# Kernel tuning notes

Measured on AMD Instinct MI355X. Metric: run time of the kernel, lower is better.

## Reference

```python
import jax, jax.numpy as jnp
import numpy as np

B, TX, DA, DS, H = 64, 2048, 256, 256, 50

def setup_inputs() -> dict:
    key = jax.random.key(0)
    k1, k2, k3, k4 = jax.random.split(key, 4)
    a = jax.random.normal(k1, (B, TX, DA), dtype=jnp.float32)
    s = jax.random.normal(k2, (B, DS), dtype=jnp.float32)
    # Dense(50, relu) params on concat dim (DA+DS)
    W1 = jax.random.normal(k3, (DA + DS, H), dtype=jnp.float32) / np.sqrt(DA + DS)
    b1 = jnp.zeros((H,), dtype=jnp.float32)
    # Dense(1, tanh) params
    W2 = jax.random.normal(k4, (H, 1), dtype=jnp.float32) / np.sqrt(H)
    b2 = jnp.zeros((1,), dtype=jnp.float32)
    return {"a": a, "s": s, "W1": W1, "b1": b1, "W2": W2, "b2": b2}

def reference(a, s, W1, b1, W2, b2):
    # repeat s along time: [B, Tx, Ds]
    s_rep = jnp.broadcast_to(s[:, None, :], (a.shape[0], a.shape[1], s.shape[-1]))
    x = jnp.concatenate([a, s_rep], axis=-1)              # [B, Tx, Da+Ds]
    h = jax.nn.relu(jnp.einsum('btc,ch->bth', x, W1) + b1)  # [B, Tx, 50]
    e = jnp.tanh(jnp.einsum('bth,ho->bto', h, W2) + b2)     # [B, Tx, 1]
    alphas = jax.nn.softmax(e, axis=1)                     # softmax over time
    # Dot(axes=1): contract the time axis -> [B, 1, Da]
    context = jnp.einsum('bto,btd->bod', alphas, a)
    return context
```

## Files before the change

### kernel.cpp

```cpp
#include <hip/hip_runtime.h>

#define B_ 64
#define TX_ 2048
#define DA_ 256
#define DS_ 256
#define H_ 50

typedef __attribute__((ext_vector_type(4))) float f32x4;
typedef __attribute__((ext_vector_type(8))) short short8;

__device__ __forceinline__ unsigned short f2bf(float x) {
  unsigned int u = __builtin_bit_cast(unsigned int, x);
  u += 0x7FFFu + ((u >> 16) & 1u);
  return (unsigned short)(u >> 16);
}
__device__ __forceinline__ float bf2f(unsigned short h) {
  unsigned int u = ((unsigned int)h) << 16;
  return __builtin_bit_cast(float, u);
}

#define WS_NUM 0
#define WS_DEN 16384
#define WS_C   16448
#define WS_W2  20544
#define WS_B   20608

__global__ __launch_bounds__(256) void prep_kernel(
    const float* __restrict__ s, const float* __restrict__ W1,
    const float* __restrict__ b1, const float* __restrict__ W2,
    float* __restrict__ ws)
{
  const int b = blockIdx.x;
  const int t = threadIdx.x;
  float* num = ws + WS_NUM;
  float* den = ws + WS_DEN;
  float* cws = ws + WS_C;
  float* w2p = ws + WS_W2;
  unsigned short* wsB = (unsigned short*)(ws + WS_B);

  num[b * 256 + t] = 0.0f;
  if (t == 0) den[b] = 0.0f;

  {
    const int h4 = t >> 2, kq = t & 3;
    float cp = 0.0f;
    if (h4 < H_) {
      const float* srow = s + b * DS_;
      #pragma unroll 8
      for (int k = kq * 64; k < kq * 64 + 64; ++k)
        cp += srow[k] * W1[(size_t)(DA_ + k) * H_ + h4];
    }
    cp += __shfl_down(cp, 1);
    cp += __shfl_down(cp, 2);
    if (kq == 0) cws[b * 64 + h4] = (h4 < H_) ? (cp + b1[h4]) : 0.0f;
  }
  if (b == 0 && t < 64) w2p[t] = (t < H_) ? W2[t] : 0.0f;

  #pragma unroll
  for (int ii = 0; ii < 2; ++ii) {
    const int idx = (b * 256 + t) * 2 + ii;
    const int j = idx & 7;
    const int l = (idx >> 3) & 63;
    const int nt = (idx >> 9) & 3;
    const int term = (idx >> 11) & 1;
    const int c = idx >> 12;
    const int k = c * 32 + (l >> 4) * 8 + j;
    const int n = nt * 16 + (l & 15);
    const float wv = (n < H_) ? W1[(size_t)k * H_ + n] : 0.0f;
    const unsigned short hi = f2bf(wv);
    const unsigned short val = term == 0 ? hi : f2bf(wv - bf2f(hi));
    wsB[((size_t)((c * 2 + term) * 4 + nt)) * 512 + l * 8 + j] = val;
  }
}

__global__ __launch_bounds__(256) void fused_kernel(
    const float* __restrict__ a, const float* __restrict__ ws_f,
    const float* __restrict__ b2, float* __restrict__ num,
    float* __restrict__ den)
{
  __shared__ float tile[16384];
  __shared__ float w_sh[64];

  const int t = threadIdx.x;
  const int l = t & 63;
  const int w = __builtin_amdgcn_readfirstlane(t >> 6);
  const int blk = blockIdx.x;
  const int b = blk >> 5;
  const long R0 = (long)blk * 64;

  const float* cws = ws_f + WS_C;
  const float* w2p = ws_f + WS_W2;
  const unsigned short* wsB = (const unsigned short*)(ws_f + WS_B);

  float cv[4], w2v[4];
  #pragma unroll
  for (int nt = 0; nt < 4; ++nt) {
    const int n = nt * 16 + (l & 15);
    cv[nt] = cws[b * 64 + n];
    w2v[nt] = w2p[n];
  }
  const float b2v = b2[0];

  #define STAGE(c)                                                             \
    {                                                                          \
      _Pragma("unroll")                                                        \
      for (int i = 0; i < 2; ++i) {                                            \
        const int slot = w * 2 + i;                                            \
        const int row = slot * 8 + (l >> 3);                                   \
        const long gbyte = (R0 + row) * 1024 + (c) * 128 +                     \
                           (((l & 7) ^ ((l >> 3) & 7)) * 16);                  \
        __builtin_amdgcn_global_load_lds(                                      \
            (const __attribute__((address_space(1))) void*)((const char*)a +   \
                                                            gbyte),            \
            (__attribute__((address_space(3))) void*)&tile[(c)*2048 +          \
                                                           slot * 256],        \
            16, 0, 0);                                                         \
      }                                                                        \
    }

  STAGE(0);
  STAGE(1);

  short8 Bh[2][4], Bl[2][4];
  {
    const short8* Bp = (const short8*)wsB;
    #pragma unroll
    for (int nt = 0; nt < 4; ++nt) {
      Bh[0][nt] = Bp[nt * 64 + l];
      Bl[0][nt] = Bp[(4 + nt) * 64 + l];
    }
  }

  f32x4 acc[4];
  #pragma unroll
  for (int nt = 0; nt < 4; ++nt) acc[nt] = (f32x4){0.f, 0.f, 0.f, 0.f};

  #pragma unroll
  for (int c = 0; c < 8; ++c) {
    if (c + 2 < 8) STAGE(c + 2);
    if (c + 1 < 8) {
      const short8* Bp = (const short8*)(wsB + (size_t)(c + 1) * 4096);
      #pragma unroll
      for (int nt = 0; nt < 4; ++nt) {
        Bh[(c + 1) & 1][nt] = Bp[nt * 64 + l];
        Bl[(c + 1) & 1][nt] = Bp[(4 + nt) * 64 + l];
      }
    }
    if (c < 6)       asm volatile("s_waitcnt vmcnt(10)" ::: "memory");
    else if (c == 6) asm volatile("s_waitcnt vmcnt(8)" ::: "memory");
    else             asm volatile("s_waitcnt vmcnt(0)" ::: "memory");
    __builtin_amdgcn_sched_barrier(0);

    const int row = w * 16 + (l & 15);
    const int mask = (l & 7) << 4;
    const int obase = (l >> 4) * 32;
    const char* tb = (const char*)tile + (size_t)c * 8192 + row * 128;
    const float4 v0 = *(const float4*)(tb + (obase ^ mask));
    const float4 v1 = *(const float4*)(tb + ((obase + 16) ^ mask));
    float av[8] = {v0.x, v0.y, v0.z, v0.w, v1.x, v1.y, v1.z, v1.w};
    short8 Ah, Al;
    #pragma unroll
    for (int j = 0; j < 8; ++j) {
      const unsigned short hi = f2bf(av[j]);
      Ah[j] = (short)hi;
      Al[j] = (short)f2bf(av[j] - bf2f(hi));
    }

    #pragma unroll
    for (int nt = 0; nt < 4; ++nt) {
      acc[nt] = __builtin_amdgcn_mfma_f32_16x16x32_bf16(Ah, Bh[c & 1][nt], acc[nt], 0, 0, 0);
      acc[nt] = __builtin_amdgcn_mfma_f32_16x16x32_bf16(Ah, Bl[c & 1][nt], acc[nt], 0, 0, 0);
      acc[nt] = __builtin_amdgcn_mfma_f32_16x16x32_bf16(Al, Bh[c & 1][nt], acc[nt], 0, 0, 0);
    }
  }

  #pragma unroll
  for (int r = 0; r < 4; ++r) {
    float e = 0.0f;
    #pragma unroll
    for (int nt = 0; nt < 4; ++nt)
      e += fmaxf(acc[nt][r] + cv[nt], 0.0f) * w2v[nt];
    e += __shfl_xor(e, 1);
    e += __shfl_xor(e, 2);
    e += __shfl_xor(e, 4);
    e += __shfl_xor(e, 8);
    if ((l & 15) == 0)
      w_sh[w * 16 + (l >> 4) * 4 + r] = __expf(tanhf(e + b2v));
  }
  __syncthreads();

  if (t < 64) {
    float v = w_sh[t];
    #pragma unroll
    for (int off = 32; off > 0; off >>= 1) v += __shfl_xor(v, off);
    if (t == 0) atomicAdd(&den[b], v);
  }

  {
    const int cc = t >> 5, col = t & 31;
    const char* tb = (const char*)tile + (size_t)cc * 8192;
    float sum = 0.0f;
    #pragma unroll 8
    for (int r = 0; r < 64; ++r) {
      const float av = *(const float*)(tb + r * 128 + ((col * 4) ^ ((r & 7) << 4)));
      sum += w_sh[r] * av;
    }
    atomicAdd(&num[b * 256 + t], sum);
  }
  #undef STAGE
}

__global__ __launch_bounds__(256) void finish_kernel(
    const float* __restrict__ ws_f, float* __restrict__ out)
{
  const int b = blockIdx.x;
  const int t = threadIdx.x;
  out[b * 256 + t] = ws_f[WS_NUM + b * 256 + t] / ws_f[WS_DEN + b];
}

extern "C" void kernel_launch(void* const* d_in, const int* in_sizes, int n_in,
                              void* d_out, int out_size, void* d_ws, size_t ws_size,
                              hipStream_t stream) {
  const float* a  = (const float*)d_in[0];
  const float* s  = (const float*)d_in[1];
  const float* W1 = (const float*)d_in[2];
  const float* b1 = (const float*)d_in[3];
  const float* W2 = (const float*)d_in[4];
  const float* b2 = (const float*)d_in[5];
  float* out = (float*)d_out;
  float* ws  = (float*)d_ws;

  prep_kernel<<<dim3(B_), dim3(256), 0, stream>>>(s, W1, b1, W2, ws);
  fused_kernel<<<dim3(2048), dim3(256), 0, stream>>>(
      a, ws, b2, ws + WS_NUM, ws + WS_DEN);
  finish_kernel<<<dim3(B_), dim3(256), 0, stream>>>(ws, out);
}
```

Baseline: 56.83 us.

## Shrink LDS footprint with a double-buffered ring and bf16 context tile for occupancy

Replaces the full 64KB fp32 tile of `a` with a two-slot staging ring and a separate bf16 copy of the tile (the rounded high halves). That copy is reused for the weighted time-sum. Launch bounds now request 3 blocks per CU. The context reduction becomes per-wave partial sums combined through LDS, and tanh is computed via exp. Prefetch depth drops from two chunks ahead to one, and the context now uses bf16-rounded activations, which lowers accuracy.

```diff
diff --git a/kernel.cpp b/kernel.cpp
--- a/kernel.cpp
+++ b/kernel.cpp
@@ -17,6 +17,15 @@
 __device__ __forceinline__ float bf2f(unsigned short h) {
   unsigned int u = ((unsigned int)h) << 16;
   return __builtin_bit_cast(float, u);
+}
+__device__ __forceinline__ unsigned bitf(float x) {
+  return __builtin_bit_cast(unsigned, x);
+}
+__device__ __forceinline__ unsigned pack_hi(float x, float y) {
+  return __builtin_amdgcn_perm(bitf(y), bitf(x), 0x07060302);
+}
+__device__ __forceinline__ float trunc_bf(float x) {
+  return __builtin_bit_cast(float, bitf(x) & 0xFFFF0000u);
 }
 
 #define WS_NUM 0
@@ -73,13 +82,14 @@
   }
 }
 
-__global__ __launch_bounds__(256) void fused_kernel(
+__global__ __launch_bounds__(256, 3) void fused_kernel(
     const float* __restrict__ a, const float* __restrict__ ws_f,
     const float* __restrict__ b2, float* __restrict__ num,
     float* __restrict__ den)
 {
-  __shared__ float tile[16384];
-  __shared__ float w_sh[64];
+  __shared__ float ring[2][2048];
+  __shared__ unsigned short bt[64][256];
+  __shared__ float partial[4][256];
 
   const int t = threadIdx.x;
   const int l = t & 63;
@@ -106,21 +116,18 @@
       _Pragma("unroll")                                                        \
       for (int i = 0; i < 2; ++i) {                                            \
         const int slot = w * 2 + i;                                            \
-        const int row = slot * 8 + (l >> 3);                                   \
-        const long gbyte = (R0 + row) * 1024 + (c) * 128 +                     \
+        const long gbyte = (R0 + slot * 8 + (l >> 3)) * 1024 + (c) * 128 +     \
                            (((l & 7) ^ ((l >> 3) & 7)) * 16);                  \
         __builtin_amdgcn_global_load_lds(                                      \
             (const __attribute__((address_space(1))) void*)((const char*)a +   \
                                                             gbyte),            \
-            (__attribute__((address_space(3))) void*)&tile[(c)*2048 +          \
-                                                           slot * 256],        \
+            (__attribute__((address_space(3))) void*)&ring[(c) & 1]            \
+                                                         [slot * 256],         \
             16, 0, 0);                                                         \
       }                                                                        \
     }
 
   STAGE(0);
-  STAGE(1);
-
   short8 Bh[2][4], Bl[2][4];
   {
     const short8* Bp = (const short8*)wsB;
@@ -135,10 +142,14 @@
   #pragma unroll
   for (int nt = 0; nt < 4; ++nt) acc[nt] = (f32x4){0.f, 0.f, 0.f, 0.f};
 
+  const int row = w * 16 + (l & 15);
+  const int mask = (l & 7) << 4;
+  const int obase = (l >> 4) * 32;
+
   #pragma unroll
   for (int c = 0; c < 8; ++c) {
-    if (c + 2 < 8) STAGE(c + 2);
     if (c + 1 < 8) {
+      STAGE(c + 1);
       const short8* Bp = (const short8*)(wsB + (size_t)(c + 1) * 4096);
       #pragma unroll
       for (int nt = 0; nt < 4; ++nt) {
@@ -146,25 +157,27 @@
         Bl[(c + 1) & 1][nt] = Bp[(4 + nt) * 64 + l];
       }
     }
-    if (c < 6)       asm volatile("s_waitcnt vmcnt(10)" ::: "memory");
-    else if (c == 6) asm volatile("s_waitcnt vmcnt(8)" ::: "memory");
-    else             asm volatile("s_waitcnt vmcnt(0)" ::: "memory");
+    if (c < 7) asm volatile("s_waitcnt vmcnt(10)" ::: "memory");
+    else       asm volatile("s_waitcnt vmcnt(0)" ::: "memory");
     __builtin_amdgcn_sched_barrier(0);
 
-    const int row = w * 16 + (l & 15);
-    const int mask = (l & 7) << 4;
-    const int obase = (l >> 4) * 32;
-    const char* tb = (const char*)tile + (size_t)c * 8192 + row * 128;
+    const char* tb = (const char*)&ring[c & 1][0] + row * 128;
     const float4 v0 = *(const float4*)(tb + (obase ^ mask));
     const float4 v1 = *(const float4*)(tb + ((obase + 16) ^ mask));
-    float av[8] = {v0.x, v0.y, v0.z, v0.w, v1.x, v1.y, v1.z, v1.w};
-    short8 Ah, Al;
-    #pragma unroll
-    for (int j = 0; j < 8; ++j) {
-      const unsigned short hi = f2bf(av[j]);
-      Ah[j] = (short)hi;
-      Al[j] = (short)f2bf(av[j] - bf2f(hi));
-    }
+    const float av[8] = {v0.x, v0.y, v0.z, v0.w, v1.x, v1.y, v1.z, v1.w};
+
+    unsigned hu[4], lu[4];
+    #pragma unroll
+    for (int p = 0; p < 4; ++p) {
+      const float x = av[2 * p], y = av[2 * p + 1];
+      hu[p] = pack_hi(x, y);
+      lu[p] = pack_hi(x - trunc_bf(x), y - trunc_bf(y));
+    }
+    const short8 Ah = __builtin_bit_cast(short8, *(uint4*)hu);
+    const short8 Al = __builtin_bit_cast(short8, *(uint4*)lu);
+
+    *(short8*)((char*)&bt[row][0] +
+               ((c * 64 + (l >> 4) * 16) ^ mask)) = Ah;
 
     #pragma unroll
     for (int nt = 0; nt < 4; ++nt) {
@@ -173,7 +186,9 @@
       acc[nt] = __builtin_amdgcn_mfma_f32_16x16x32_bf16(Al, Bh[c & 1][nt], acc[nt], 0, 0, 0);
     }
   }
-
+  #undef STAGE
+
+  float wr[4];
   #pragma unroll
   for (int r = 0; r < 4; ++r) {
     float e = 0.0f;
@@ -184,30 +199,37 @@
     e += __shfl_xor(e, 2);
     e += __shfl_xor(e, 4);
     e += __shfl_xor(e, 8);
-    if ((l & 15) == 0)
-      w_sh[w * 16 + (l >> 4) * 4 + r] = __expf(tanhf(e + b2v));
-  }
+    e += b2v;
+    const float th = 1.0f - 2.0f / (__expf(2.0f * e) + 1.0f);
+    wr[r] = __expf(th);
+  }
+
+  f32x4 csum = (f32x4){0.f, 0.f, 0.f, 0.f};
+  float wsum = 0.0f;
+  #pragma unroll
+  for (int r = 0; r < 16; ++r) {
+    const float wv = __shfl(wr[r & 3], (r >> 2) * 16);
+    wsum += wv;
+    const int grow = w * 16 + r;
+    const uint2 u = *(const uint2*)((const char*)&bt[grow][0] +
+                                    ((8 * l) ^ ((grow & 7) << 4)));
+    const float f0 = __builtin_bit_cast(float, u.x << 16);
+    const float f1 = __builtin_bit_cast(float, u.x & 0xFFFF0000u);
+    const float f2 = __builtin_bit_cast(float, u.y << 16);
+    const float f3 = __builtin_bit_cast(float, u.y & 0xFFFF0000u);
+    csum.x += wv * f0;
+    csum.y += wv * f1;
+    csum.z += wv * f2;
+    csum.w += wv * f3;
+  }
+  if (l == 0) atomicAdd(&den[b], wsum);
+  *(f32x4*)&partial[w][4 * l] = csum;
   __syncthreads();
 
-  if (t < 64) {
-    float v = w_sh[t];
-    #pragma unroll
-    for (int off = 32; off > 0; off >>= 1) v += __shfl_xor(v, off);
-    if (t == 0) atomicAdd(&den[b], v);
-  }
-
   {
-    const int cc = t >> 5, col = t & 31;
-    const char* tb = (const char*)tile + (size_t)cc * 8192;
-    float sum = 0.0f;
-    #pragma unroll 8
-    for (int r = 0; r < 64; ++r) {
-      const float av = *(const float*)(tb + r * 128 + ((col * 4) ^ ((r & 7) << 4)));
-      sum += w_sh[r] * av;
-    }
-    atomicAdd(&num[b * 256 + t], sum);
-  }
-  #undef STAGE
+    const float v = partial[0][t] + partial[1][t] + partial[2][t] + partial[3][t];
+    atomicAdd(&num[b * 256 + t], v);
+  }
 }
 
 __global__ __launch_bounds__(256) void finish_kernel(
```

Result: slower. 93.30 us (+64.2%).
